# Kernel tuning notes

Hardware: AMD Instinct MI355X
Metric: run time of the kernel (lower is better)

## Reference

```python
import jax, jax.numpy as jnp
import numpy as np

B, N_I, N_H1, N_H2, N_H3, N_H4 = 4096, 1024, 1024, 1024, 2048, 1024


def _linear_params(key, n_out, n_in, gain=1.0):
    kw, kb = jax.random.split(key)
    # xavier_uniform on weight, torch default uniform bias ~ U(-1/sqrt(n_in), 1/sqrt(n_in))
    limit = gain * np.sqrt(6.0 / (n_in + n_out))
    W = jax.random.uniform(kw, (n_out, n_in), jnp.float32, -limit, limit)
    bl = 1.0 / np.sqrt(n_in)
    b = jax.random.uniform(kb, (n_out,), jnp.float32, -bl, bl)
    return W, b


def setup_inputs() -> dict:
    key = jax.random.key(0)
    ks = jax.random.split(key, 16)
    inp = {
        "X": jax.random.normal(ks[0], (B, N_I), jnp.float32),
        "hidden1": jax.random.normal(ks[1], (B, N_H1), jnp.float32),
        "hidden2": jax.random.normal(ks[2], (B, N_H2), jnp.float32),
        "cell1": jax.random.normal(ks[3], (B, N_H1), jnp.float32),
        "cell2": jax.random.normal(ks[4], (B, N_H2), jnp.float32),
    }
    # LSTM1 gates: Linear(n_i + n_h1, n_h1)
    inp["Wf1"], inp["bf1"] = _linear_params(ks[5], N_H1, N_I + N_H1, 1.0)
    inp["Wi1"], inp["bi1"] = _linear_params(ks[6], N_H1, N_I + N_H1, 1.0)
    inp["Wc1"], inp["bc1"] = _linear_params(ks[7], N_H1, N_I + N_H1, 5.0 / 3.0)
    inp["Wo1"], inp["bo1"] = _linear_params(ks[8], N_H1, N_I + N_H1, 1.0)
    # LSTM2 gates: Linear(n_h1 + n_h2, n_h2)
    inp["Wf2"], inp["bf2"] = _linear_params(ks[9], N_H2, N_H1 + N_H2, 1.0)
    inp["Wi2"], inp["bi2"] = _linear_params(ks[10], N_H2, N_H1 + N_H2, 1.0)
    inp["Wc2"], inp["bc2"] = _linear_params(ks[11], N_H2, N_H1 + N_H2, 5.0 / 3.0)
    inp["Wo2"], inp["bo2"] = _linear_params(ks[12], N_H2, N_H1 + N_H2, 1.0)
    # MLP head
    inp["W3"], inp["b3"] = _linear_params(ks[13], N_H3, N_H2, np.sqrt(2.0))
    inp["W4"], inp["b4"] = _linear_params(ks[14], N_H4, N_H3, 1.0)
    return inp


def _lstm_cell(x, h, c, Wf, bf, Wi, bi, Wc, bc, Wo, bo):
    z = jnp.concatenate([x, h], axis=1)           # [B, n_i + n_h]
    f = jax.nn.sigmoid(z @ Wf.T + bf)
    i = jax.nn.sigmoid(z @ Wi.T + bi)
    cand = jnp.tanh(z @ Wc.T + bc)
    o = jax.nn.sigmoid(z @ Wo.T + bo)
    h_new = o * jnp.tanh(cand)                    # NOTE: double tanh, faithful to source
    c_new = f * c + cand * i
    return h_new, c_new


def reference(X, hidden1, hidden2, cell1, cell2,
              Wf1, bf1, Wi1, bi1, Wc1, bc1, Wo1, bo1,
              Wf2, bf2, Wi2, bi2, Wc2, bc2, Wo2, bo2,
              W3, b3, W4, b4):
    h1, c1 = _lstm_cell(X, hidden1, cell1, Wf1, bf1, Wi1, bi1, Wc1, bc1, Wo1, bo1)
    h2, c2 = _lstm_cell(h1, hidden2, cell2, Wf2, bf2, Wi2, bi2, Wc2, bc2, Wo2, bo2)
    out3 = jax.nn.relu(h2 @ W3.T + b3)
    out = out3 @ W4.T + b4
    return (out, h1, h2, c1, c2)
```

## Files before the change

### kernel.cpp

```cpp
#include <hip/hip_runtime.h>
#include <hip/hip_bf16.h>
#include <stdint.h>

typedef unsigned short u16;
typedef __bf16 bf16x8 __attribute__((ext_vector_type(8)));
typedef float f32x4 __attribute__((ext_vector_type(4)));
typedef float f32x8 __attribute__((ext_vector_type(8)));

#define BM 128
#define BN 128
#define BK 64

struct SegArgs {
  const u16* W[4];
  const float* b[4];
  void* out[4];
  int act[4];
  int bf16out[4];
};

struct LstmArgs {
  const u16* W[4];
  const float* b[4];
  const float* cold;
  float* h;
  float* c;
  u16*   hb;
};

__device__ __forceinline__ float bf2f(u16 u) {
  union { unsigned int i; float f; } v; v.i = ((unsigned int)u) << 16; return v.f;
}
__device__ __forceinline__ u16 f2bf(float f) {
  union { float f; unsigned int i; } v; v.f = f;
  return (u16)((v.i + 0x7fffu + ((v.i >> 16) & 1u)) >> 16);
}
__device__ __forceinline__ uint4 cvt8(f32x8 v) {
  uint4 r;
  r.x = (unsigned)f2bf(v[0]) | ((unsigned)f2bf(v[1]) << 16);
  r.y = (unsigned)f2bf(v[2]) | ((unsigned)f2bf(v[3]) << 16);
  r.z = (unsigned)f2bf(v[4]) | ((unsigned)f2bf(v[5]) << 16);
  r.w = (unsigned)f2bf(v[6]) | ((unsigned)f2bf(v[7]) << 16);
  return r;
}
__device__ __forceinline__ float actf(float x, int act) {
  if (act == 1) return 1.0f / (1.0f + __expf(-x));
  if (act == 2) {
    float xc = fminf(fmaxf(x, -15.0f), 15.0f);
    float e = __expf(2.0f * xc);
    return (e - 1.0f) / (e + 1.0f);
  }
  if (act == 3) return fmaxf(x, 0.0f);
  return x;
}

struct CvtArgs { const float* src[10]; u16* dst[10]; };
__global__ void cvt_f2b(CvtArgs a) {
  const float* s = a.src[blockIdx.y];
  u16* d = a.dst[blockIdx.y];
  int i0 = (blockIdx.x * 256 + threadIdx.x) * 8;
  f32x8 v = *(const f32x8*)(s + i0);
  *(uint4*)(d + i0) = cvt8(v);
}

__global__ __launch_bounds__(256, 2) void gemm_lstm2(
    const u16* __restrict__ A0, const u16* __restrict__ A1, int KA0, int K,
    LstmArgs La)
{
  __shared__ u16 smem[2 * 8192];
  u16* As = smem;
  u16* Bs = smem + 8192;

  const int tid  = threadIdx.x;
  const int lane = tid & 63;
  const int wave = tid >> 6;
  const int mBlock = blockIdx.x * BM;
  const int nTile  = blockIdx.y;
  const int colBase32 = nTile * 32;
  const int wm = wave & 1, wn = wave >> 1;

  const int rsub = tid >> 3;
  const int kc   = (tid & 7) ^ (rsub & 7);
  const u16* pA[4];
  const u16* pB[4];
#pragma unroll
  for (int it = 0; it < 4; ++it) {
    pB[it] = La.W[it] + (size_t)(colBase32 + rsub) * (size_t)K + kc * 8;
    pA[it] = A0 + (size_t)(mBlock + it * 32 + rsub) * (size_t)KA0 + kc * 8;
  }

  const f32x4 zero = {0.f, 0.f, 0.f, 0.f};
  f32x4 acc[4][4];
#pragma unroll
  for (int i = 0; i < 4; ++i)
#pragma unroll
    for (int j = 0; j < 4; ++j) acc[i][j] = zero;

  for (int kb = 0; kb < K; kb += BK) {
    if (kb == KA0) {
#pragma unroll
      for (int it = 0; it < 4; ++it)
        pA[it] = A1 + (size_t)(mBlock + it * 32 + rsub) * (size_t)(K - KA0) + kc * 8;
    }
#pragma unroll
    for (int it = 0; it < 4; ++it) {
      u16* dA = &As[(it * 256 + wave * 64) * 8];
      u16* dB = &Bs[(it * 256 + wave * 64) * 8];
      __builtin_amdgcn_global_load_lds((void*)pA[it], (void*)dA, 16, 0, 0);
      __builtin_amdgcn_global_load_lds((void*)pB[it], (void*)dB, 16, 0, 0);
      pA[it] += BK; pB[it] += BK;
    }
    __syncthreads();

#pragma unroll
    for (int ko = 0; ko < 2; ++ko) {
      bf16x8 af[4], bfr[4];
      int kcb = ko * 4 + (lane >> 4);
      int p = kcb ^ (lane & 7);
#pragma unroll
      for (int t = 0; t < 4; ++t) {
        int ml = wm * 64 + t * 16 + (lane & 15);
        af[t]  = *(const bf16x8*)&As[(ml * 8 + p) * 8];
        int nl = wn * 64 + t * 16 + (lane & 15);
        bfr[t] = *(const bf16x8*)&Bs[(nl * 8 + p) * 8];
      }
#pragma unroll
      for (int tm = 0; tm < 4; ++tm)
#pragma unroll
        for (int tn = 0; tn < 4; ++tn)
          acc[tm][tn] = __builtin_amdgcn_mfma_f32_16x16x32_bf16(af[tm], bfr[tn], acc[tm][tn], 0, 0, 0);
    }
    __syncthreads();
  }

  const int cl = lane & 15;
  const int q4 = (lane >> 4) * 4;
#pragma unroll
  for (int tn = 0; tn < 4; ++tn) {
    const int g = wn * 2 + (tn >> 1);
    const float* bg = (tn >> 1) ? (wn ? La.b[3] : La.b[1])
                                : (wn ? La.b[2] : La.b[0]);
    const bool isT = (wn == 1) && ((tn >> 1) == 0);
    const int col = (tn & 1) * 16 + cl;
    float bv = bg[colBase32 + col];
#pragma unroll
    for (int tm = 0; tm < 4; ++tm) {
      const int rbase = wm * 64 + tm * 16 + q4;
#pragma unroll
      for (int r = 0; r < 4; ++r) {
        float x = acc[tm][tn][r] + bv;
        float a;
        if (isT) {
          float xc = fminf(fmaxf(x, -15.f), 15.f);
          float e = __expf(2.f * xc);
          a = (e - 1.f) / (e + 1.f);
        } else {
          a = 1.f / (1.f + __expf(-x));
        }
        int row = rbase + r;
        smem[g * 4096 + row * 32 + (((col >> 3) ^ ((row >> 2) & 3)) << 3) + (col & 7)] = f2bf(a);
      }
    }
  }
  __syncthreads();

  {
    const int rowL = tid >> 1;
    const int hf   = tid & 1;
    const int xr   = (rowL >> 2) & 3;
    union GU { uint4 v; u16 u[8]; };
    GU gu[4][2];
#pragma unroll
    for (int g = 0; g < 4; ++g)
#pragma unroll
      for (int jj = 0; jj < 2; ++jj) {
        int ch = (hf * 2 + jj) ^ xr;
        gu[g][jj].v = *(const uint4*)&smem[g * 4096 + rowL * 32 + ch * 8];
      }
    size_t base = (size_t)(mBlock + rowL) * 1024 + colBase32 + hf * 16;
    f32x8 cA = *(const f32x8*)(La.cold + base);
    f32x8 cB = *(const f32x8*)(La.cold + base + 8);
    f32x8 H0, H1, C0, C1;
#pragma unroll
    for (int j = 0; j < 8; ++j) {
      float f  = bf2f(gu[0][0].u[j]);
      float iv = bf2f(gu[1][0].u[j]);
      float cd = bf2f(gu[2][0].u[j]);
      float o  = bf2f(gu[3][0].u[j]);
      float cn = f * cA[j] + cd * iv;
      float e  = __expf(2.0f * cd);
      float th = (e - 1.0f) / (e + 1.0f);
      H0[j] = o * th;
      C0[j] = cn;
    }
#pragma unroll
    for (int j = 0; j < 8; ++j) {
      float f  = bf2f(gu[0][1].u[j]);
      float iv = bf2f(gu[1][1].u[j]);
      float cd = bf2f(gu[2][1].u[j]);
      float o  = bf2f(gu[3][1].u[j]);
      float cn = f * cB[j] + cd * iv;
      float e  = __expf(2.0f * cd);
      float th = (e - 1.0f) / (e + 1.0f);
      H1[j] = o * th;
      C1[j] = cn;
    }
    *(f32x8*)(La.h + base)     = H0;
    *(f32x8*)(La.h + base + 8) = H1;
    *(f32x8*)(La.c + base)     = C0;
    *(f32x8*)(La.c + base + 8) = C1;
    *(uint4*)(La.hb + base)     = cvt8(H0);
    *(uint4*)(La.hb + base + 8) = cvt8(H1);
  }
}

__global__ __launch_bounds__(256, 2) void gemm_bt(
    const u16* __restrict__ A0, const u16* __restrict__ A1, int KA0, int K,
    SegArgs segs, int tileShift, int ldOut)
{
  __shared__ u16 As[BM * BK];
  __shared__ u16 Bs[BN * BK];

  const int tid  = threadIdx.x;
  const int lane = tid & 63;
  const int wave = tid >> 6;
  const int mBlock = blockIdx.x * BM;
  const int seg   = blockIdx.y >> tileShift;
  const int nTile = blockIdx.y & ((1 << tileShift) - 1);

  const u16* Wp = segs.W[seg];
  const int wm = wave & 1, wn = wave >> 1;

  const f32x4 zero = {0.f, 0.f, 0.f, 0.f};
  f32x4 acc[4][4];
#pragma unroll
  for (int i = 0; i < 4; ++i)
#pragma unroll
    for (int j = 0; j < 4; ++j) acc[i][j] = zero;

  for (int kb = 0; kb < K; kb += BK) {
    const u16* Aseg; int ka; int ldA;
    if (kb < KA0) { Aseg = A0; ka = kb;       ldA = KA0; }
    else          { Aseg = A1; ka = kb - KA0; ldA = K - KA0; }

#pragma unroll
    for (int it = 0; it < 4; ++it) {
      int s = it * 256 + tid;
      int m = s >> 3;
      int p = s & 7;
      int kc = p ^ (m & 7);
      const u16* srcA = Aseg + (size_t)(mBlock + m) * (size_t)ldA + (ka + kc * 8);
      const u16* srcB = Wp + (size_t)(nTile * BN + m) * (size_t)K + (kb + kc * 8);
      u16* dA = &As[(it * 256 + wave * 64) * 8];
      u16* dB = &Bs[(it * 256 + wave * 64) * 8];
      __builtin_amdgcn_global_load_lds((void*)srcA, (void*)dA, 16, 0, 0);
      __builtin_amdgcn_global_load_lds((void*)srcB, (void*)dB, 16, 0, 0);
    }
    __syncthreads();

#pragma unroll
    for (int ko = 0; ko < 2; ++ko) {
      bf16x8 af[4], bfr[4];
      int kcb = ko * 4 + (lane >> 4);
      int p = kcb ^ (lane & 7);
#pragma unroll
      for (int t = 0; t < 4; ++t) {
        int ml = wm * 64 + t * 16 + (lane & 15);
        af[t]  = *(const bf16x8*)&As[(ml * 8 + p) * 8];
        int nl = wn * 64 + t * 16 + (lane & 15);
        bfr[t] = *(const bf16x8*)&Bs[(nl * 8 + p) * 8];
      }
#pragma unroll
      for (int tm = 0; tm < 4; ++tm)
#pragma unroll
        for (int tn = 0; tn < 4; ++tn)
          acc[tm][tn] = __builtin_amdgcn_mfma_f32_16x16x32_bf16(af[tm], bfr[tn], acc[tm][tn], 0, 0, 0);
    }
    __syncthreads();
  }

  const float* bp = segs.b[seg];
  const int act = segs.act[seg];
  const int isBf = segs.bf16out[seg];
  u16*   opb = (u16*)segs.out[seg];
  float* opf = (float*)segs.out[seg];
  const int q  = lane >> 4;
  const int cl = lane & 15;
#pragma unroll
  for (int tn = 0; tn < 4; ++tn) {
    int col = nTile * BN + wn * 64 + tn * 16 + cl;
    float bv = bp[col];
#pragma unroll
    for (int tm = 0; tm < 4; ++tm) {
      int row = mBlock + wm * 64 + tm * 16 + q * 4;
#pragma unroll
      for (int r = 0; r < 4; ++r) {
        float v = actf(acc[tm][tn][r] + bv, act);
        size_t idx = (size_t)(row + r) * (size_t)ldOut + col;
        if (isBf) opb[idx] = f2bf(v); else opf[idx] = v;
      }
    }
  }
}

extern "C" void kernel_launch(void* const* d_in, const int* in_sizes, int n_in,
                              void* d_out, int out_size, void* d_ws, size_t ws_size,
                              hipStream_t stream)
{
  const size_t P   = 4096ull * 1024ull;
  const size_t C2M = 2097152ull;

  const float* X   = (const float*)d_in[0];
  const float* h1i = (const float*)d_in[1];
  const float* h2i = (const float*)d_in[2];
  const float* c1i = (const float*)d_in[3];
  const float* c2i = (const float*)d_in[4];
  const float* Wf1 = (const float*)d_in[5];  const float* bf1_ = (const float*)d_in[6];
  const float* Wi1 = (const float*)d_in[7];  const float* bi1_ = (const float*)d_in[8];
  const float* Wc1 = (const float*)d_in[9];  const float* bc1_ = (const float*)d_in[10];
  const float* Wo1 = (const float*)d_in[11]; const float* bo1_ = (const float*)d_in[12];
  const float* Wf2 = (const float*)d_in[13]; const float* bf2_ = (const float*)d_in[14];
  const float* Wi2 = (const float*)d_in[15]; const float* bi2_ = (const float*)d_in[16];
  const float* Wc2 = (const float*)d_in[17]; const float* bc2_ = (const float*)d_in[18];
  const float* Wo2 = (const float*)d_in[19]; const float* bo2_ = (const float*)d_in[20];
  const float* W3  = (const float*)d_in[21]; const float* b3_  = (const float*)d_in[22];
  const float* W4  = (const float*)d_in[23]; const float* b4_  = (const float*)d_in[24];

  float* out = (float*)d_out;
  float* h1  = out + P;
  float* h2  = out + 2 * P;
  float* c1  = out + 3 * P;
  float* c2  = out + 4 * P;

  char* ws = (char*)d_ws;
  u16* Areg  = (u16*)(ws + (32ull << 20));
  u16* Breg  = (u16*)(ws + (48ull << 20));
  u16* Creg  = (u16*)(ws + (56ull << 20));
  u16* Ereg  = (u16*)(ws + (64ull << 20));
  u16* Freg  = (u16*)(ws + (72ull << 20));

  dim3 blk(256, 1, 1);

  CvtArgs ca;
  ca.src[0]=Wf1;        ca.dst[0]=Areg;
  ca.src[1]=Wi1;        ca.dst[1]=Areg + C2M;
  ca.src[2]=Wc1;        ca.dst[2]=Areg + 2*C2M;
  ca.src[3]=Wo1;        ca.dst[3]=Areg + 3*C2M;
  ca.src[4]=X;          ca.dst[4]=Breg;
  ca.src[5]=X + C2M;    ca.dst[5]=Breg + C2M;
  ca.src[6]=h1i;        ca.dst[6]=Creg;
  ca.src[7]=h1i + C2M;  ca.dst[7]=Creg + C2M;
  ca.src[8]=W3;         ca.dst[8]=Freg;
  ca.src[9]=W4;         ca.dst[9]=Freg + C2M;
  cvt_f2b<<<dim3(1024, 10, 1), blk, 0, stream>>>(ca);

  LstmArgs l1;
  l1.W[0]=Areg; l1.W[1]=Areg+C2M; l1.W[2]=Areg+2*C2M; l1.W[3]=Areg+3*C2M;
  l1.b[0]=bf1_; l1.b[1]=bi1_; l1.b[2]=bc1_; l1.b[3]=bo1_;
  l1.cold=c1i; l1.h=h1; l1.c=c1; l1.hb=Ereg;
  gemm_lstm2<<<dim3(32,32,1), blk, 0, stream>>>(Breg, Creg, 1024, 2048, l1);

  CvtArgs cb;
  cb.src[0]=Wf2;        cb.dst[0]=Areg;
  cb.src[1]=Wi2;        cb.dst[1]=Areg + C2M;
  cb.src[2]=Wc2;        cb.dst[2]=Areg + 2*C2M;
  cb.src[3]=Wo2;        cb.dst[3]=Areg + 3*C2M;
  cb.src[4]=h2i;        cb.dst[4]=Breg;
  cb.src[5]=h2i + C2M;  cb.dst[5]=Breg + C2M;
  cvt_f2b<<<dim3(1024, 6, 1), blk, 0, stream>>>(cb);

  LstmArgs l2;
  l2.W[0]=Areg; l2.W[1]=Areg+C2M; l2.W[2]=Areg+2*C2M; l2.W[3]=Areg+3*C2M;
  l2.b[0]=bf2_; l2.b[1]=bi2_; l2.b[2]=bc2_; l2.b[3]=bo2_;
  l2.cold=c2i; l2.h=h2; l2.c=c2; l2.hb=Creg;
  gemm_lstm2<<<dim3(32,32,1), blk, 0, stream>>>(Ereg, Breg, 1024, 2048, l2);

  SegArgs s3;
  for (int g = 0; g < 4; ++g) { s3.W[g]=Freg; s3.b[g]=b3_; s3.out[g]=Areg; s3.act[g]=3; s3.bf16out[g]=1; }
  gemm_bt<<<dim3(32,16,1), blk, 0, stream>>>(Creg, (const u16*)nullptr, 1024, 1024, s3, 4, 2048);

  SegArgs s4;
  for (int g = 0; g < 4; ++g) { s4.W[g]=Freg+C2M; s4.b[g]=b4_; s4.out[g]=out; s4.act[g]=0; s4.bf16out[g]=0; }
  gemm_bt<<<dim3(32,8,1), blk, 0, stream>>>(Areg, (const u16*)nullptr, 2048, 2048, s4, 3, 1024);
}
```

Before: 468.8 us.

## Fold layer-2 and MLP weight conversion into the layer-1 LSTM GEMM launch

Drops the separate conversion launch before the second LSTM cell. Its work (LSTM2 weights, hidden2, and now W3/W4) is handed to an extra row of 32 blocks in the first LSTM GEMM grid, which grid-stride over the copy and exit. The workspace layout is split into distinct regions so the converted buffers no longer alias the live ones. This saves one launch and lets the fp32-to-bf16 conversion overlap the GEMM, but only 32 blocks handle about 16M elements, which could lengthen the tail of that kernel.

Result: slower. 634.8 us (+35.4%).

```diff
diff --git a/kernel.cpp b/kernel.cpp
--- a/kernel.cpp
+++ b/kernel.cpp
@@ -28,6 +28,8 @@
   u16*   hb;
 };
 
+struct CvtW { const float* src[8]; u16* dst[8]; int n; };
+
 __device__ __forceinline__ float bf2f(u16 u) {
   union { unsigned int i; float f; } v; v.i = ((unsigned int)u) << 16; return v.f;
 }
@@ -65,17 +67,33 @@
 
 __global__ __launch_bounds__(256, 2) void gemm_lstm2(
     const u16* __restrict__ A0, const u16* __restrict__ A1, int KA0, int K,
-    LstmArgs La)
+    LstmArgs La, CvtW cw, int cvtRows)
 {
   __shared__ u16 smem[2 * 8192];
   u16* As = smem;
   u16* Bs = smem + 8192;
 
   const int tid  = threadIdx.x;
+
+  if (blockIdx.y < (unsigned)cvtRows) {
+    const int nb  = gridDim.x * cvtRows;
+    const int bid = blockIdx.y * gridDim.x + blockIdx.x;
+    const int total = cw.n << 18;
+    for (int g = bid * 256 + tid; g < total; g += nb * 256) {
+      int region = g >> 18;
+      int within = g & 0x3FFFF;
+      const float* s = cw.src[region] + (size_t)within * 8;
+      u16* d = cw.dst[region] + (size_t)within * 8;
+      f32x8 v = *(const f32x8*)s;
+      *(uint4*)d = cvt8(v);
+    }
+    return;
+  }
+
   const int lane = tid & 63;
   const int wave = tid >> 6;
   const int mBlock = blockIdx.x * BM;
-  const int nTile  = blockIdx.y;
+  const int nTile  = blockIdx.y - cvtRows;
   const int colBase32 = nTile * 32;
   const int wm = wave & 1, wn = wave >> 1;
 
@@ -333,53 +351,61 @@
   float* c2  = out + 4 * P;
 
   char* ws = (char*)d_ws;
-  u16* Areg  = (u16*)(ws + (32ull << 20));
-  u16* Breg  = (u16*)(ws + (48ull << 20));
-  u16* Creg  = (u16*)(ws + (56ull << 20));
-  u16* Ereg  = (u16*)(ws + (64ull << 20));
-  u16* Freg  = (u16*)(ws + (72ull << 20));
+  u16* W1b  = (u16*)ws;
+  u16* W2b  = (u16*)(ws + (16ull << 20));
+  u16* W3b  = (u16*)(ws + (32ull << 20));
+  u16* W4b  = (u16*)(ws + (36ull << 20));
+  u16* Xb   = (u16*)(ws + (40ull << 20));
+  u16* h1ib = (u16*)(ws + (48ull << 20));
+  u16* h2ib = (u16*)(ws + (56ull << 20));
+  u16* h1b  = (u16*)(ws + (64ull << 20));
+  u16* h2b  = (u16*)(ws + (72ull << 20));
+  u16* out3b = W1b;
 
   dim3 blk(256, 1, 1);
 
   CvtArgs ca;
-  ca.src[0]=Wf1;        ca.dst[0]=Areg;
-  ca.src[1]=Wi1;        ca.dst[1]=Areg + C2M;
-  ca.src[2]=Wc1;        ca.dst[2]=Areg + 2*C2M;
-  ca.src[3]=Wo1;        ca.dst[3]=Areg + 3*C2M;
-  ca.src[4]=X;          ca.dst[4]=Breg;
-  ca.src[5]=X + C2M;    ca.dst[5]=Breg + C2M;
-  ca.src[6]=h1i;        ca.dst[6]=Creg;
-  ca.src[7]=h1i + C2M;  ca.dst[7]=Creg + C2M;
-  ca.src[8]=W3;         ca.dst[8]=Freg;
-  ca.src[9]=W4;         ca.dst[9]=Freg + C2M;
-  cvt_f2b<<<dim3(1024, 10, 1), blk, 0, stream>>>(ca);
+  ca.src[0]=Wf1;        ca.dst[0]=W1b;
+  ca.src[1]=Wi1;        ca.dst[1]=W1b + C2M;
+  ca.src[2]=Wc1;        ca.dst[2]=W1b + 2*C2M;
+  ca.src[3]=Wo1;        ca.dst[3]=W1b + 3*C2M;
+  ca.src[4]=X;          ca.dst[4]=Xb;
+  ca.src[5]=X + C2M;    ca.dst[5]=Xb + C2M;
+  ca.src[6]=h1i;        ca.dst[6]=h1ib;
+  ca.src[7]=h1i + C2M;  ca.dst[7]=h1ib + C2M;
+  ca.src[8]=nullptr;    ca.dst[8]=nullptr;
+  ca.src[9]=nullptr;    ca.dst[9]=nullptr;
+  cvt_f2b<<<dim3(1024, 8, 1), blk, 0, stream>>>(ca);
 
   LstmArgs l1;
-  l1.W[0]=Areg; l1.W[1]=Areg+C2M; l1.W[2]=Areg+2*C2M; l1.W[3]=Areg+3*C2M;
+  l1.W[0]=W1b; l1.W[1]=W1b+C2M; l1.W[2]=W1b+2*C2M; l1.W[3]=W1b+3*C2M;
   l1.b[0]=bf1_; l1.b[1]=bi1_; l1.b[2]=bc1_; l1.b[3]=bo1_;
-  l1.cold=c1i; l1.h=h1; l1.c=c1; l1.hb=Ereg;
-  gemm_lstm2<<<dim3(32,32,1), blk, 0, stream>>>(Breg, Creg, 1024, 2048, l1);
-
-  CvtArgs cb;
-  cb.src[0]=Wf2;        cb.dst[0]=Areg;
-  cb.src[1]=Wi2;        cb.dst[1]=Areg + C2M;
-  cb.src[2]=Wc2;        cb.dst[2]=Areg + 2*C2M;
-  cb.src[3]=Wo2;        cb.dst[3]=Areg + 3*C2M;
-  cb.src[4]=h2i;        cb.dst[4]=Breg;
-  cb.src[5]=h2i + C2M;  cb.dst[5]=Breg + C2M;
-  cvt_f2b<<<dim3(1024, 6, 1), blk, 0, stream>>>(cb);
+  l1.cold=c1i; l1.h=h1; l1.c=c1; l1.hb=h1b;
+  CvtW cw1;
+  cw1.src[0]=Wf2;       cw1.dst[0]=W2b;
+  cw1.src[1]=Wi2;       cw1.dst[1]=W2b + C2M;
+  cw1.src[2]=Wc2;       cw1.dst[2]=W2b + 2*C2M;
+  cw1.src[3]=Wo2;       cw1.dst[3]=W2b + 3*C2M;
+  cw1.src[4]=h2i;       cw1.dst[4]=h2ib;
+  cw1.src[5]=h2i + C2M; cw1.dst[5]=h2ib + C2M;
+  cw1.src[6]=W3;        cw1.dst[6]=W3b;
+  cw1.src[7]=W4;        cw1.dst[7]=W4b;
+  cw1.n = 8;
+  gemm_lstm2<<<dim3(32, 33, 1), blk, 0, stream>>>(Xb, h1ib, 1024, 2048, l1, cw1, 1);
 
   LstmArgs l2;
-  l2.W[0]=Areg; l2.W[1]=Areg+C2M; l2.W[2]=Areg+2*C2M; l2.W[3]=Areg+3*C2M;
+  l2.W[0]=W2b; l2.W[1]=W2b+C2M; l2.W[2]=W2b+2*C2M; l2.W[3]=W2b+3*C2M;
   l2.b[0]=bf2_; l2.b[1]=bi2_; l2.b[2]=bc2_; l2.b[3]=bo2_;
-  l2.cold=c2i; l2.h=h2; l2.c=c2; l2.hb=Creg;
-  gemm_lstm2<<<dim3(32,32,1), blk, 0, stream>>>(Ereg, Breg, 1024, 2048, l2);
+  l2.cold=c2i; l2.h=h2; l2.c=c2; l2.hb=h2b;
+  CvtW cw0; cw0.n = 0;
+  for (int i = 0; i < 8; ++i) { cw0.src[i]=nullptr; cw0.dst[i]=nullptr; }
+  gemm_lstm2<<<dim3(32, 32, 1), blk, 0, stream>>>(h1b, h2ib, 1024, 2048, l2, cw0, 0);
 
   SegArgs s3;
-  for (int g = 0; g < 4; ++g) { s3.W[g]=Freg; s3.b[g]=b3_; s3.out[g]=Areg; s3.act[g]=3; s3.bf16out[g]=1; }
-  gemm_bt<<<dim3(32,16,1), blk, 0, stream>>>(Creg, (const u16*)nullptr, 1024, 1024, s3, 4, 2048);
+  for (int g = 0; g < 4; ++g) { s3.W[g]=W3b; s3.b[g]=b3_; s3.out[g]=out3b; s3.act[g]=3; s3.bf16out[g]=1; }
+  gemm_bt<<<dim3(32,16,1), blk, 0, stream>>>(h2b, (const u16*)nullptr, 1024, 1024, s3, 4, 2048);
 
   SegArgs s4;
-  for (int g = 0; g < 4; ++g) { s4.W[g]=Freg+C2M; s4.b[g]=b4_; s4.out[g]=out; s4.act[g]=0; s4.bf16out[g]=0; }
-  gemm_bt<<<dim3(32,8,1), blk, 0, stream>>>(Areg, (const u16*)nullptr, 2048, 2048, s4, 3, 1024);
-}
+  for (int g = 0; g < 4; ++g) { s4.W[g]=W4b; s4.b[g]=b4_; s4.out[g]=out; s4.act[g]=0; s4.bf16out[g]=0; }
+  gemm_bt<<<dim3(32,8,1), blk, 0, stream>>>(out3b, (const u16*)nullptr, 2048, 2048, s4, 3, 1024);
+}
```
